# Kernel optimization log

Measured on AMD Instinct MI355X. Metric: run time of the kernel, lower is better.

The kernel has to match this reference:

```python
import math
import jax, jax.numpy as jnp
import numpy as np

S, H, D = 2048, 16, 128

def setup_inputs() -> dict:
    key = jax.random.key(0)
    kq, kk, kv = jax.random.split(key, 3)
    Q = jax.random.normal(kq, (S, H, D), dtype=jnp.float32)
    K = jax.random.normal(kk, (S, H, D), dtype=jnp.float32)
    V = jax.random.normal(kv, (S, H, D), dtype=jnp.float32)
    return {"Q": Q, "K": K, "V": V}

def reference(Q, K, V):
    s, h, d = Q.shape
    # scores[i,h,j] = sum_d Q[i,h,d] * K[j,h,d]  (torch einsum 'ijk,kjl->ijl' with K.T)
    scores = jnp.einsum('ihd,jhd->ihj', Q, K) / np.float32(math.sqrt(d))
    # causal mask: y -= triu(inf, 1) broadcast over heads -> -inf above diagonal
    causal = jnp.triu(jnp.ones((s, s), dtype=bool), k=1)  # [S, S]
    scores = jnp.where(causal[:, None, :], -jnp.inf, scores)
    attn = jax.nn.softmax(scores, axis=2)  # softmax over keys (dim 2)
    # out[i,h,d] = sum_j attn[i,h,j] * V[j,h,d]
    return jnp.einsum('ihj,jhd->ihd', attn, V)
```

## Files before the change

### kernel.cpp

```cpp
#include <hip/hip_runtime.h>
#include <hip/hip_bf16.h>

#define S_LEN 2048
#define NH 16
#define HD 128
#define KBLK 64
#define SM_BOUND 14.0f

typedef short short8 __attribute__((ext_vector_type(8)));
typedef float f32x4 __attribute__((ext_vector_type(4)));

__device__ __forceinline__ ushort f2bf(float f) {
  union { float f; unsigned u; } v; v.f = f;
  unsigned u = v.u;
  return (ushort)((u + 0x7fffu + ((u >> 16) & 1u)) >> 16);
}

#define GLDS(gp, lp)                                                      \
  __builtin_amdgcn_global_load_lds(                                       \
      (const __attribute__((address_space(1))) void*)(gp),                \
      (__attribute__((address_space(3))) void*)(lp), 16, 0, 0)

__global__ __launch_bounds__(256)
void prep(const float* __restrict__ Kg, const float* __restrict__ Vg,
          ushort* __restrict__ Kb, ushort* __restrict__ Vb) {
  __shared__ ushort lt[64 * HD];
  const int tid = threadIdx.x;
  const int h = blockIdx.x & 15;
  const int j0 = (blockIdx.x >> 4) * 64;

#pragma unroll
  for (int it = 0; it < 8; ++it) {
    int flat = it * 256 + tid;
    int r = flat >> 5, d4 = (flat & 31) * 4;
    float4 v = *(const float4*)(Kg + ((size_t)(j0 + r) * NH + h) * HD + d4);
    ushort4 b;
    b.x = f2bf(v.x); b.y = f2bf(v.y); b.z = f2bf(v.z); b.w = f2bf(v.w);
    *(ushort4*)(Kb + ((size_t)h * S_LEN + j0 + r) * HD + d4) = b;
  }
#pragma unroll
  for (int it = 0; it < 8; ++it) {
    int flat = it * 256 + tid;
    int r = flat >> 5, d4 = (flat & 31) * 4;
    float4 v = *(const float4*)(Vg + ((size_t)(j0 + r) * NH + h) * HD + d4);
    ushort4 b;
    b.x = f2bf(v.x); b.y = f2bf(v.y); b.z = f2bf(v.z); b.w = f2bf(v.w);
    *(ushort4*)(&lt[r * 128 + (d4 ^ ((r & 7) << 3))]) = b;
  }
  __syncthreads();
  const int d = tid >> 1, half = tid & 1;
  ushort vals[32];
#pragma unroll
  for (int j = 0; j < 32; ++j) {
    int jjj = half * 32 + j;
    vals[j] = lt[jjj * 128 + (d ^ ((jjj & 7) << 3))];
  }
  ushort* dst = Vb + ((size_t)h * HD + d) * S_LEN + j0 + half * 32;
#pragma unroll
  for (int q = 0; q < 4; ++q) {
    short8 w;
#pragma unroll
    for (int e = 0; e < 8; ++e) w[e] = (short)vals[q * 8 + e];
    *(short8*)(dst + q * 8) = w;
  }
}

__global__ __launch_bounds__(512, 2)
void attn_fwd6(const float* __restrict__ Qg, const ushort* __restrict__ Kb,
               const ushort* __restrict__ Vb, float* __restrict__ Og) {
  __shared__ ushort lds_k[3][KBLK * HD];
  __shared__ ushort lds_vt[3][HD * KBLK];
  __shared__ ushort lds_p[64 * 64];
  __shared__ float  lsc[2][4][2][16];

  const int tid = threadIdx.x;
  const int l   = tid & 63;
  const int wv  = tid >> 6;
  const int qf  = wv >> 2;
  const int kh  = wv & 3;
  const int dh  = wv & 3;
  const int lr  = l & 15;
  const int lg  = l >> 4;

  const int bid = blockIdx.x;
  const int h   = bid & 15;
  const int jj  = bid >> 4;
  const int qtA = 31 - jj;
  const int qbA = qtA * 64, qbB = jj * 64;

  const ushort* khp = Kb + (size_t)h * S_LEN * HD;
  const ushort* vhp = Vb + (size_t)h * HD * S_LEN;

  const int b0 = tid, b1 = 512 + tid;
  const int r0 = b0 >> 4, r1 = b1 >> 4;
  const int koff0 = r0 * 128 + (((b0 & 15) ^ (r0 & 7)) << 3);
  const int koff1 = r1 * 128 + (((b1 & 15) ^ (r1 & 7)) << 3);
  const int dd0 = b0 >> 3, dd1 = b1 >> 3;
  const int voff0 = dd0 * S_LEN + (((b0 & 7) ^ (dd0 & 7)) << 3);
  const int voff1 = dd1 * S_LEN + (((b1 & 7) ^ (dd1 & 7)) << 3);

  auto stage = [&](int buf, int kc) {
    const ushort* kbase = khp + (size_t)kc * (KBLK * HD);
    GLDS(kbase + koff0, &lds_k[buf][tid * 8]);
    GLDS(kbase + koff1, &lds_k[buf][4096 + tid * 8]);
    const ushort* vbase = vhp + (size_t)kc * KBLK;
    GLDS(vbase + voff0, &lds_vt[buf][tid * 8]);
    GLDS(vbase + voff1, &lds_vt[buf][4096 + tid * 8]);
  };

  const float scale = 0.08838834764831845f;
  short8 qfrA[2][4], qfrB[2][4];
  auto loadQ = [&](short8 (&dst)[2][4], int qb) {
#pragma unroll
    for (int qc = 0; qc < 2; ++qc) {
      const float* qsrc = Qg + ((size_t)(qb + qf * 32 + qc * 16 + lr) * NH + h) * HD;
#pragma unroll
      for (int dk = 0; dk < 4; ++dk) {
        float4 a = *(const float4*)(qsrc + dk * 32 + lg * 8);
        float4 b2 = *(const float4*)(qsrc + dk * 32 + lg * 8 + 4);
        short8 f;
        f[0] = (short)f2bf(a.x * scale);  f[1] = (short)f2bf(a.y * scale);
        f[2] = (short)f2bf(a.z * scale);  f[3] = (short)f2bf(a.w * scale);
        f[4] = (short)f2bf(b2.x * scale); f[5] = (short)f2bf(b2.y * scale);
        f[6] = (short)f2bf(b2.z * scale); f[7] = (short)f2bf(b2.w * scale);
        dst[qc][dk] = f;
      }
    }
  };
  loadQ(qfrA, qbA);
  loadQ(qfrB, qbB);

  f32x4 oacc[2][2];
#pragma unroll
  for (int qc = 0; qc < 2; ++qc)
#pragma unroll
    for (int dt = 0; dt < 2; ++dt) oacc[qc][dt] = (f32x4){0.f, 0.f, 0.f, 0.f};
  float l_run[2] = {0.f, 0.f};

  auto epilogue = [&](int qb) {
    float t0 = l_run[0], t1 = l_run[1];
    t0 += __shfl_xor(t0, 16, 64); t0 += __shfl_xor(t0, 32, 64);
    t1 += __shfl_xor(t1, 16, 64); t1 += __shfl_xor(t1, 32, 64);
    if (lg == 0) { lsc[qf][kh][0][lr] = t0; lsc[qf][kh][1][lr] = t1; }
    __syncthreads();
    float inv[2][4];
#pragma unroll
    for (int qc = 0; qc < 2; ++qc)
#pragma unroll
      for (int i = 0; i < 4; ++i) {
        int q15 = lg * 4 + i;
        float sl = (lsc[qf][0][qc][q15] + lsc[qf][1][qc][q15]) +
                   (lsc[qf][2][qc][q15] + lsc[qf][3][qc][q15]);
        inv[qc][i] = 1.0f / sl;
      }
#pragma unroll
    for (int qc = 0; qc < 2; ++qc)
#pragma unroll
      for (int dt = 0; dt < 2; ++dt)
#pragma unroll
        for (int i = 0; i < 4; ++i) {
          int qg = qb + qf * 32 + qc * 16 + lg * 4 + i;
          Og[((size_t)qg * NH + h) * HD + dh * 32 + dt * 16 + lr] =
              oacc[qc][dt][i] * inv[qc][i];
        }
  };

  stage(0, 0);
  stage(1, 1);

  for (int g = 0; g < 33; ++g) {
    if (g == 32) { asm volatile("s_waitcnt vmcnt(0)" ::: "memory"); }
    else         { asm volatile("s_waitcnt vmcnt(4)" ::: "memory"); }
    asm volatile("s_barrier" ::: "memory");
    if (g + 2 < 33) {
      int t = g + 2;
      stage(t % 3, (t <= qtA) ? t : (t - qtA - 1));
    }
    const int bI = g % 3;
    const ushort* lk = lds_k[bI];
    const ushort* lv = lds_vt[bI];
    const bool tB = (g > qtA);
    const int kc = tB ? (g - qtA - 1) : g;
    const int qb = tB ? qbB : qbA;

    f32x4 s0 = (f32x4){0.f, 0.f, 0.f, 0.f};
    f32x4 s1 = (f32x4){0.f, 0.f, 0.f, 0.f};
    const int krow = kh * 16 + lr;
    __builtin_amdgcn_s_setprio(1);
    if (!tB) {
#pragma unroll
      for (int dk = 0; dk < 4; ++dk) {
        short8 kf = *(const short8*)&lk[krow * 128 + ((dk * 32 + lg * 8) ^ ((lr & 7) << 3))];
        s0 = __builtin_amdgcn_mfma_f32_16x16x32_bf16(kf, qfrA[0][dk], s0, 0, 0, 0);
        s1 = __builtin_amdgcn_mfma_f32_16x16x32_bf16(kf, qfrA[1][dk], s1, 0, 0, 0);
      }
    } else {
#pragma unroll
      for (int dk = 0; dk < 4; ++dk) {
        short8 kf = *(const short8*)&lk[krow * 128 + ((dk * 32 + lg * 8) ^ ((lr & 7) << 3))];
        s0 = __builtin_amdgcn_mfma_f32_16x16x32_bf16(kf, qfrB[0][dk], s0, 0, 0, 0);
        s1 = __builtin_amdgcn_mfma_f32_16x16x32_bf16(kf, qfrB[1][dk], s1, 0, 0, 0);
      }
    }
    __builtin_amdgcn_s_setprio(0);

    float p0[4], p1[4];
    if (g == qtA || g == 32) {
      const int qg0 = qb + qf * 32 + lr;
#pragma unroll
      for (int i = 0; i < 4; ++i) {
        int kg = kc * 64 + kh * 16 + lg * 4 + i;
        float e0 = __expf(s0[i] - SM_BOUND);
        float e1 = __expf(s1[i] - SM_BOUND);
        p0[i] = (kg > qg0) ? 0.f : e0;
        p1[i] = (kg > qg0 + 16) ? 0.f : e1;
      }
    } else {
#pragma unroll
      for (int i = 0; i < 4; ++i) {
        p0[i] = __expf(s0[i] - SM_BOUND);
        p1[i] = __expf(s1[i] - SM_BOUND);
      }
    }
    l_run[0] += (p0[0] + p0[1]) + (p0[2] + p0[3]);
    l_run[1] += (p1[0] + p1[1]) + (p1[2] + p1[3]);

    {
      int q0 = qf * 32 + lr;
      int q1 = q0 + 16;
      unsigned w;
      asm("v_cvt_pk_bf16_f32 %0, %1, %2" : "=v"(w) : "v"(p0[0]), "v"(p0[1]));
      *(unsigned*)&lds_p[q0 * 64 + ((kh * 16 + lg * 4 + 0) ^ ((q0 & 7) << 3))] = w;
      asm("v_cvt_pk_bf16_f32 %0, %1, %2" : "=v"(w) : "v"(p0[2]), "v"(p0[3]));
      *(unsigned*)&lds_p[q0 * 64 + ((kh * 16 + lg * 4 + 2) ^ ((q0 & 7) << 3))] = w;
      asm("v_cvt_pk_bf16_f32 %0, %1, %2" : "=v"(w) : "v"(p1[0]), "v"(p1[1]));
      *(unsigned*)&lds_p[q1 * 64 + ((kh * 16 + lg * 4 + 0) ^ ((q1 & 7) << 3))] = w;
      asm("v_cvt_pk_bf16_f32 %0, %1, %2" : "=v"(w) : "v"(p1[2]), "v"(p1[3]));
      *(unsigned*)&lds_p[q1 * 64 + ((kh * 16 + lg * 4 + 2) ^ ((q1 & 7) << 3))] = w;
    }
    asm volatile("s_waitcnt lgkmcnt(0)" ::: "memory");
    asm volatile("s_barrier" ::: "memory");
    __builtin_amdgcn_sched_barrier(0);

    short8 pa0[2], pa1[2];
    {
      int q0 = qf * 32 + lr;
      int q1 = q0 + 16;
      pa0[0] = *(const short8*)&lds_p[q0 * 64 + ((lg * 8) ^ ((q0 & 7) << 3))];
      pa0[1] = *(const short8*)&lds_p[q0 * 64 + ((32 + lg * 8) ^ ((q0 & 7) << 3))];
      pa1[0] = *(const short8*)&lds_p[q1 * 64 + ((lg * 8) ^ ((q1 & 7) << 3))];
      pa1[1] = *(const short8*)&lds_p[q1 * 64 + ((32 + lg * 8) ^ ((q1 & 7) << 3))];
    }
    __builtin_amdgcn_s_setprio(1);
#pragma unroll
    for (int dt = 0; dt < 2; ++dt) {
      int d = dh * 32 + dt * 16 + lr;
#pragma unroll
      for (int ks = 0; ks < 2; ++ks) {
        short8 vf = *(const short8*)&lv[d * 64 + ((ks * 32 + lg * 8) ^ ((d & 7) << 3))];
        oacc[0][dt] = __builtin_amdgcn_mfma_f32_16x16x32_bf16(pa0[ks], vf, oacc[0][dt], 0, 0, 0);
        oacc[1][dt] = __builtin_amdgcn_mfma_f32_16x16x32_bf16(pa1[ks], vf, oacc[1][dt], 0, 0, 0);
      }
    }
    __builtin_amdgcn_s_setprio(0);

    if (g == qtA) {
      epilogue(qbA);
#pragma unroll
      for (int qc = 0; qc < 2; ++qc)
#pragma unroll
        for (int dt = 0; dt < 2; ++dt) oacc[qc][dt] = (f32x4){0.f, 0.f, 0.f, 0.f};
      l_run[0] = 0.f; l_run[1] = 0.f;
    }
  }
  epilogue(qbB);
}

__global__ __launch_bounds__(256, 2)
void attn_fwd_fb(const float* __restrict__ Qg, const float* __restrict__ Kg,
                 const float* __restrict__ Vg, float* __restrict__ Og) {
  __shared__ ushort lds_k[KBLK * HD];
  __shared__ ushort lds_vt[HD * KBLK];
  __shared__ ushort lds_p[4][16 * KBLK];

  const int tid = threadIdx.x;
  const int l  = tid & 63;
  const int wv = tid >> 6;
  const int lr = l & 15;
  const int lg = l >> 4;

  const int bid = blockIdx.x;
  const int h  = bid & 15;
  const int qi = bid >> 4;
  const int qt = (qi < 16) ? (31 - 2 * qi) : (2 * (qi - 16));
  const int qbase = qt * 64;

  short8 qf[4];
  {
    const float* qsrc = Qg + ((size_t)(qbase + wv * 16 + lr) * NH + h) * HD;
#pragma unroll
    for (int dk = 0; dk < 4; ++dk) {
      float4 a = *(const float4*)(qsrc + dk * 32 + lg * 8);
      float4 b = *(const float4*)(qsrc + dk * 32 + lg * 8 + 4);
      short8 f;
      f[0] = (short)f2bf(a.x); f[1] = (short)f2bf(a.y);
      f[2] = (short)f2bf(a.z); f[3] = (short)f2bf(a.w);
      f[4] = (short)f2bf(b.x); f[5] = (short)f2bf(b.y);
      f[6] = (short)f2bf(b.z); f[7] = (short)f2bf(b.w);
      qf[dk] = f;
    }
  }

  f32x4 oacc[8];
#pragma unroll
  for (int dt = 0; dt < 8; ++dt) oacc[dt] = (f32x4){0.f, 0.f, 0.f, 0.f};
  float l_run[4] = {0.f, 0.f, 0.f, 0.f};

  const float scale = 0.08838834764831845f;
  const int nch = qt + 1;

  for (int c = 0; c < nch; ++c) {
    const int k0 = c * KBLK;
    __syncthreads();
#pragma unroll
    for (int it = 0; it < 8; ++it) {
      int flat = (it * 256 + tid) * 4;
      int r = flat >> 7, d = flat & 127;
      float4 v = *(const float4*)(Kg + ((size_t)(k0 + r) * NH + h) * HD + d);
      int idx = (r * 128 + d) ^ ((r & 7) << 3);
      ushort4 b4;
      b4.x = f2bf(v.x); b4.y = f2bf(v.y); b4.z = f2bf(v.z); b4.w = f2bf(v.w);
      *(ushort4*)&lds_k[idx] = b4;
    }
#pragma unroll
    for (int it = 0; it < 8; ++it) {
      int d0 = wv * 32 + it * 4;
      float4 v = *(const float4*)(Vg + ((size_t)(k0 + l) * NH + h) * HD + d0);
      lds_vt[((d0 + 0) * 64 + l) ^ (((d0 + 0) & 7) << 3)] = f2bf(v.x);
      lds_vt[((d0 + 1) * 64 + l) ^ (((d0 + 1) & 7) << 3)] = f2bf(v.y);
      lds_vt[((d0 + 2) * 64 + l) ^ (((d0 + 2) & 7) << 3)] = f2bf(v.z);
      lds_vt[((d0 + 3) * 64 + l) ^ (((d0 + 3) & 7) << 3)] = f2bf(v.w);
    }
    __syncthreads();

    f32x4 sacc[4];
#pragma unroll
    for (int kc = 0; kc < 4; ++kc) {
      sacc[kc] = (f32x4){0.f, 0.f, 0.f, 0.f};
#pragma unroll
      for (int dk = 0; dk < 4; ++dk) {
        int row = kc * 16 + lr;
        int idx = (row * 128 + dk * 32 + lg * 8) ^ ((row & 7) << 3);
        short8 kf = *(const short8*)&lds_k[idx];
        sacc[kc] = __builtin_amdgcn_mfma_f32_16x16x32_bf16(qf[dk], kf, sacc[kc], 0, 0, 0);
      }
    }

    float p[4][4];
    if (c == qt) {
#pragma unroll
      for (int i = 0; i < 4; ++i) {
        int qg = qbase + wv * 16 + lg * 4 + i;
#pragma unroll
        for (int kc = 0; kc < 4; ++kc) {
          float e = __expf(sacc[kc][i] * scale - SM_BOUND);
          p[kc][i] = (k0 + kc * 16 + lr > qg) ? 0.f : e;
        }
      }
    } else {
#pragma unroll
      for (int i = 0; i < 4; ++i)
#pragma unroll
        for (int kc = 0; kc < 4; ++kc)
          p[kc][i] = __expf(sacc[kc][i] * scale - SM_BOUND);
    }
#pragma unroll
    for (int i = 0; i < 4; ++i)
      l_run[i] += (p[0][i] + p[1][i]) + (p[2][i] + p[3][i]);

#pragma unroll
    for (int kc = 0; kc < 4; ++kc)
#pragma unroll
      for (int i = 0; i < 4; ++i) {
        int row = lg * 4 + i, col = kc * 16 + lr;
        lds_p[wv][(row * 64 + col) ^ ((row & 7) << 3)] = f2bf(p[kc][i]);
      }
    asm volatile("s_waitcnt lgkmcnt(0)" ::: "memory");
    __builtin_amdgcn_sched_barrier(0);

    short8 pa[2];
#pragma unroll
    for (int ks = 0; ks < 2; ++ks) {
      int idx = (lr * 64 + ks * 32 + lg * 8) ^ ((lr & 7) << 3);
      pa[ks] = *(const short8*)&lds_p[wv][idx];
    }

#pragma unroll
    for (int dt = 0; dt < 8; ++dt) {
#pragma unroll
      for (int ks = 0; ks < 2; ++ks) {
        int d = dt * 16 + lr;
        int idx = (d * 64 + ks * 32 + lg * 8) ^ ((d & 7) << 3);
        short8 vf = *(const short8*)&lds_vt[idx];
        oacc[dt] = __builtin_amdgcn_mfma_f32_16x16x32_bf16(pa[ks], vf, oacc[dt], 0, 0, 0);
      }
    }
  }

#pragma unroll
  for (int mk = 1; mk <= 8; mk <<= 1)
#pragma unroll
    for (int i = 0; i < 4; ++i)
      l_run[i] += __shfl_xor(l_run[i], mk, 64);
  float inv[4];
#pragma unroll
  for (int i = 0; i < 4; ++i) inv[i] = 1.0f / l_run[i];
#pragma unroll
  for (int dt = 0; dt < 8; ++dt)
#pragma unroll
    for (int i = 0; i < 4; ++i) {
      int qg = qbase + wv * 16 + lg * 4 + i;
      Og[((size_t)qg * NH + h) * HD + dt * 16 + lr] = oacc[dt][i] * inv[i];
    }
}

extern "C" void kernel_launch(void* const* d_in, const int* in_sizes, int n_in,
                              void* d_out, int out_size, void* d_ws, size_t ws_size,
                              hipStream_t stream) {
  (void)in_sizes; (void)n_in; (void)out_size;
  const float* Q = (const float*)d_in[0];
  const float* K = (const float*)d_in[1];
  const float* V = (const float*)d_in[2];
  float* O = (float*)d_out;

  const size_t elems = (size_t)S_LEN * NH * HD;
  const size_t need = 2 * elems * sizeof(ushort);
  if (ws_size >= need) {
    ushort* Kb = (ushort*)d_ws;
    ushort* Vb = Kb + elems;
    prep<<<dim3(512), dim3(256), 0, stream>>>(K, V, Kb, Vb);
    attn_fwd6<<<dim3(256), dim3(512), 0, stream>>>(Q, Kb, Vb, O);
  } else {
    attn_fwd_fb<<<dim3(512), dim3(256), 0, stream>>>(Q, K, V, O);
  }
}
```

Baseline: 64.36 us.

## Double key block to 128 and restructure K/V staging pipeline

Raises the key block from 64 to 128 rows, so each wave computes a 32x32 score tile per step and the paired-tile loop drops from 33 to 17 iterations. K stays double-buffered in LDS while V becomes single-buffered; its next block is issued after the PV MFMAs finish, and the P scratch grows to 64x128. The aim is to cut per-iteration barrier, wait and softmax overhead and to get more MFMA work per sync. The cost is more masked work on diagonal chunks, V load latency that may no longer be hidden, and higher LDS use.

```diff
diff --git a/kernel.cpp b/kernel.cpp
--- a/kernel.cpp
+++ b/kernel.cpp
@@ -4,11 +4,13 @@
 #define S_LEN 2048
 #define NH 16
 #define HD 128
-#define KBLK 64
+#define KBLK 128
 #define SM_BOUND 14.0f
 
 typedef short short8 __attribute__((ext_vector_type(8)));
 typedef float f32x4 __attribute__((ext_vector_type(4)));
+
+#define MFMA32(a, b, c) __builtin_amdgcn_mfma_f32_16x16x32_bf16(a, b, c, 0, 0, 0)
 
 __device__ __forceinline__ ushort f2bf(float f) {
   union { float f; unsigned u; } v; v.f = f;
@@ -66,11 +68,11 @@
 }
 
 __global__ __launch_bounds__(512, 2)
-void attn_fwd6(const float* __restrict__ Qg, const ushort* __restrict__ Kb,
+void attn_fwd8(const float* __restrict__ Qg, const ushort* __restrict__ Kb,
                const ushort* __restrict__ Vb, float* __restrict__ Og) {
-  __shared__ ushort lds_k[3][KBLK * HD];
-  __shared__ ushort lds_vt[3][HD * KBLK];
-  __shared__ ushort lds_p[64 * 64];
+  __shared__ ushort lds_k[2][KBLK * HD];
+  __shared__ ushort lds_vt[HD * KBLK];
+  __shared__ ushort lds_p[64 * KBLK];
   __shared__ float  lsc[2][4][2][16];
 
   const int tid = threadIdx.x;
@@ -87,26 +89,33 @@
   const int jj  = bid >> 4;
   const int qtA = 31 - jj;
   const int qbA = qtA * 64, qbB = jj * 64;
+  const int nchA = (qtA >> 1) + 1;
+  const int nch  = 17;
 
   const ushort* khp = Kb + (size_t)h * S_LEN * HD;
   const ushort* vhp = Vb + (size_t)h * HD * S_LEN;
 
-  const int b0 = tid, b1 = 512 + tid;
-  const int r0 = b0 >> 4, r1 = b1 >> 4;
-  const int koff0 = r0 * 128 + (((b0 & 15) ^ (r0 & 7)) << 3);
-  const int koff1 = r1 * 128 + (((b1 & 15) ^ (r1 & 7)) << 3);
-  const int dd0 = b0 >> 3, dd1 = b1 >> 3;
-  const int voff0 = dd0 * S_LEN + (((b0 & 7) ^ (dd0 & 7)) << 3);
-  const int voff1 = dd1 * S_LEN + (((b1 & 7) ^ (dd1 & 7)) << 3);
-
-  auto stage = [&](int buf, int kc) {
+  int koff[4], voff[4];
+#pragma unroll
+  for (int i = 0; i < 4; ++i) {
+    int Dg = i * 512 + tid;
+    int r = Dg >> 4, gp = Dg & 15;
+    koff[i] = r * 128 + ((gp ^ (r & 7)) << 3);
+    voff[i] = r * S_LEN + ((gp ^ (r & 7)) << 3);
+  }
+  auto stageK = [&](int buf, int kc) {
     const ushort* kbase = khp + (size_t)kc * (KBLK * HD);
-    GLDS(kbase + koff0, &lds_k[buf][tid * 8]);
-    GLDS(kbase + koff1, &lds_k[buf][4096 + tid * 8]);
+#pragma unroll
+    for (int i = 0; i < 4; ++i)
+      GLDS(kbase + koff[i], &lds_k[buf][(i * 512 + tid) * 8]);
+  };
+  auto stageV = [&](int kc) {
     const ushort* vbase = vhp + (size_t)kc * KBLK;
-    GLDS(vbase + voff0, &lds_vt[buf][tid * 8]);
-    GLDS(vbase + voff1, &lds_vt[buf][4096 + tid * 8]);
+#pragma unroll
+    for (int i = 0; i < 4; ++i)
+      GLDS(vbase + voff[i], &lds_vt[(i * 512 + tid) * 8]);
   };
+  auto kc_of = [&](int g) { return (g < nchA) ? g : (g - nchA); };
 
   const float scale = 0.08838834764831845f;
   short8 qfrA[2][4], qfrB[2][4];
@@ -142,7 +151,8 @@
     t0 += __shfl_xor(t0, 16, 64); t0 += __shfl_xor(t0, 32, 64);
     t1 += __shfl_xor(t1, 16, 64); t1 += __shfl_xor(t1, 32, 64);
     if (lg == 0) { lsc[qf][kh][0][lr] = t0; lsc[qf][kh][1][lr] = t1; }
-    __syncthreads();
+    asm volatile("s_waitcnt lgkmcnt(0)" ::: "memory");
+    asm volatile("s_barrier" ::: "memory");
     float inv[2][4];
 #pragma unroll
     for (int qc = 0; qc < 2; ++qc)
@@ -163,108 +173,131 @@
           Og[((size_t)qg * NH + h) * HD + dh * 32 + dt * 16 + lr] =
               oacc[qc][dt][i] * inv[qc][i];
         }
+    asm volatile("s_barrier" ::: "memory");
   };
 
-  stage(0, 0);
-  stage(1, 1);
-
-  for (int g = 0; g < 33; ++g) {
-    if (g == 32) { asm volatile("s_waitcnt vmcnt(0)" ::: "memory"); }
-    else         { asm volatile("s_waitcnt vmcnt(4)" ::: "memory"); }
+  stageK(0, 0);
+  stageV(0);
+  stageK(1, (nchA > 1) ? 1 : 0);
+  asm volatile("s_waitcnt vmcnt(0)" ::: "memory");
+  __syncthreads();
+
+  for (int g = 0; g < nch; ++g) {
+    if (g + 1 < nch) { asm volatile("s_waitcnt vmcnt(4)" ::: "memory"); }
+    else             { asm volatile("s_waitcnt vmcnt(0)" ::: "memory"); }
     asm volatile("s_barrier" ::: "memory");
-    if (g + 2 < 33) {
-      int t = g + 2;
-      stage(t % 3, (t <= qtA) ? t : (t - qtA - 1));
-    }
-    const int bI = g % 3;
-    const ushort* lk = lds_k[bI];
-    const ushort* lv = lds_vt[bI];
-    const bool tB = (g > qtA);
-    const int kc = tB ? (g - qtA - 1) : g;
+
+    const int b = g & 1;
+    const ushort* lk = lds_k[b];
+    const bool tB = (g >= nchA);
+    const int kc = kc_of(g);
     const int qb = tB ? qbB : qbA;
-
-    f32x4 s0 = (f32x4){0.f, 0.f, 0.f, 0.f};
-    f32x4 s1 = (f32x4){0.f, 0.f, 0.f, 0.f};
-    const int krow = kh * 16 + lr;
+    const bool diag = (g == nchA - 1) || (g == nch - 1);
+
+    f32x4 s00 = (f32x4){0.f, 0.f, 0.f, 0.f};
+    f32x4 s01 = (f32x4){0.f, 0.f, 0.f, 0.f};
+    f32x4 s10 = (f32x4){0.f, 0.f, 0.f, 0.f};
+    f32x4 s11 = (f32x4){0.f, 0.f, 0.f, 0.f};
+    const int krow0 = kh * 32 + lr;
+    const int krow1 = krow0 + 16;
     __builtin_amdgcn_s_setprio(1);
     if (!tB) {
 #pragma unroll
       for (int dk = 0; dk < 4; ++dk) {
-        short8 kf = *(const short8*)&lk[krow * 128 + ((dk * 32 + lg * 8) ^ ((lr & 7) << 3))];
-        s0 = __builtin_amdgcn_mfma_f32_16x16x32_bf16(kf, qfrA[0][dk], s0, 0, 0, 0);
-        s1 = __builtin_amdgcn_mfma_f32_16x16x32_bf16(kf, qfrA[1][dk], s1, 0, 0, 0);
+        short8 kf0 = *(const short8*)&lk[krow0 * 128 + ((dk * 32 + lg * 8) ^ ((krow0 & 7) << 3))];
+        short8 kf1 = *(const short8*)&lk[krow1 * 128 + ((dk * 32 + lg * 8) ^ ((krow1 & 7) << 3))];
+        s00 = MFMA32(kf0, qfrA[0][dk], s00);
+        s01 = MFMA32(kf0, qfrA[1][dk], s01);
+        s10 = MFMA32(kf1, qfrA[0][dk], s10);
+        s11 = MFMA32(kf1, qfrA[1][dk], s11);
       }
     } else {
 #pragma unroll
       for (int dk = 0; dk < 4; ++dk) {
-        short8 kf = *(const short8*)&lk[krow * 128 + ((dk * 32 + lg * 8) ^ ((lr & 7) << 3))];
-        s0 = __builtin_amdgcn_mfma_f32_16x16x32_bf16(kf, qfrB[0][dk], s0, 0, 0, 0);
-        s1 = __builtin_amdgcn_mfma_f32_16x16x32_bf16(kf, qfrB[1][dk], s1, 0, 0, 0);
+        short8 kf0 = *(const short8*)&lk[krow0 * 128 + ((dk * 32 + lg * 8) ^ ((krow0 & 7) << 3))];
+        short8 kf1 = *(const short8*)&lk[krow1 * 128 + ((dk * 32 + lg * 8) ^ ((krow1 & 7) << 3))];
+        s00 = MFMA32(kf0, qfrB[0][dk], s00);
+        s01 = MFMA32(kf0, qfrB[1][dk], s01);
+        s10 = MFMA32(kf1, qfrB[0][dk], s10);
+        s11 = MFMA32(kf1, qfrB[1][dk], s11);
       }
     }
     __builtin_amdgcn_s_setprio(0);
 
-    float p0[4], p1[4];
-    if (g == qtA || g == 32) {
-      const int qg0 = qb + qf * 32 + lr;
+    float p[2][2][4];
+    if (diag) {
+#pragma unroll
+      for (int qc = 0; qc < 2; ++qc) {
+        int qg = qb + qf * 32 + qc * 16 + lr;
+#pragma unroll
+        for (int i = 0; i < 4; ++i) {
+          int kg0 = kc * 128 + kh * 32 + lg * 4 + i;
+          float e;
+          e = __expf((qc ? s01 : s00)[i] - SM_BOUND);
+          p[0][qc][i] = (kg0 > qg) ? 0.f : e;
+          e = __expf((qc ? s11 : s10)[i] - SM_BOUND);
+          p[1][qc][i] = (kg0 + 16 > qg) ? 0.f : e;
+        }
+      }
+    } else {
 #pragma unroll
       for (int i = 0; i < 4; ++i) {
-        int kg = kc * 64 + kh * 16 + lg * 4 + i;
-        float e0 = __expf(s0[i] - SM_BOUND);
-        float e1 = __expf(s1[i] - SM_BOUND);
-        p0[i] = (kg > qg0) ? 0.f : e0;
-        p1[i] = (kg > qg0 + 16) ? 0.f : e1;
-      }
-    } else {
-#pragma unroll
-      for (int i = 0; i < 4; ++i) {
-        p0[i] = __expf(s0[i] - SM_BOUND);
-        p1[i] = __expf(s1[i] - SM_BOUND);
-      }
-    }
-    l_run[0] += (p0[0] + p0[1]) + (p0[2] + p0[3]);
-    l_run[1] += (p1[0] + p1[1]) + (p1[2] + p1[3]);
-
-    {
-      int q0 = qf * 32 + lr;
-      int q1 = q0 + 16;
-      unsigned w;
-      asm("v_cvt_pk_bf16_f32 %0, %1, %2" : "=v"(w) : "v"(p0[0]), "v"(p0[1]));
-      *(unsigned*)&lds_p[q0 * 64 + ((kh * 16 + lg * 4 + 0) ^ ((q0 & 7) << 3))] = w;
-      asm("v_cvt_pk_bf16_f32 %0, %1, %2" : "=v"(w) : "v"(p0[2]), "v"(p0[3]));
-      *(unsigned*)&lds_p[q0 * 64 + ((kh * 16 + lg * 4 + 2) ^ ((q0 & 7) << 3))] = w;
-      asm("v_cvt_pk_bf16_f32 %0, %1, %2" : "=v"(w) : "v"(p1[0]), "v"(p1[1]));
-      *(unsigned*)&lds_p[q1 * 64 + ((kh * 16 + lg * 4 + 0) ^ ((q1 & 7) << 3))] = w;
-      asm("v_cvt_pk_bf16_f32 %0, %1, %2" : "=v"(w) : "v"(p1[2]), "v"(p1[3]));
-      *(unsigned*)&lds_p[q1 * 64 + ((kh * 16 + lg * 4 + 2) ^ ((q1 & 7) << 3))] = w;
+        p[0][0][i] = __expf(s00[i] - SM_BOUND);
+        p[0][1][i] = __expf(s01[i] - SM_BOUND);
+        p[1][0][i] = __expf(s10[i] - SM_BOUND);
+        p[1][1][i] = __expf(s11[i] - SM_BOUND);
+      }
+    }
+#pragma unroll
+    for (int qc = 0; qc < 2; ++qc)
+      l_run[qc] += ((p[0][qc][0] + p[0][qc][1]) + (p[0][qc][2] + p[0][qc][3])) +
+                   ((p[1][qc][0] + p[1][qc][1]) + (p[1][qc][2] + p[1][qc][3]));
+
+#pragma unroll
+    for (int qc = 0; qc < 2; ++qc) {
+      int q = qf * 32 + qc * 16 + lr;
+      int sw = (q & 7) << 3;
+#pragma unroll
+      for (int kcc = 0; kcc < 2; ++kcc) {
+        int kb = kh * 32 + kcc * 16 + lg * 4;
+        unsigned w;
+        asm("v_cvt_pk_bf16_f32 %0, %1, %2" : "=v"(w) : "v"(p[kcc][qc][0]), "v"(p[kcc][qc][1]));
+        *(unsigned*)&lds_p[q * 128 + ((((kb) >> 3 << 3) ^ sw) + (kb & 7))] = w;
+        asm("v_cvt_pk_bf16_f32 %0, %1, %2" : "=v"(w) : "v"(p[kcc][qc][2]), "v"(p[kcc][qc][3]));
+        *(unsigned*)&lds_p[q * 128 + ((((kb + 2) >> 3 << 3) ^ sw) + ((kb + 2) & 7))] = w;
+      }
     }
     asm volatile("s_waitcnt lgkmcnt(0)" ::: "memory");
     asm volatile("s_barrier" ::: "memory");
     __builtin_amdgcn_sched_barrier(0);
 
-    short8 pa0[2], pa1[2];
+    short8 pa0[4], pa1[4];
     {
-      int q0 = qf * 32 + lr;
-      int q1 = q0 + 16;
-      pa0[0] = *(const short8*)&lds_p[q0 * 64 + ((lg * 8) ^ ((q0 & 7) << 3))];
-      pa0[1] = *(const short8*)&lds_p[q0 * 64 + ((32 + lg * 8) ^ ((q0 & 7) << 3))];
-      pa1[0] = *(const short8*)&lds_p[q1 * 64 + ((lg * 8) ^ ((q1 & 7) << 3))];
-      pa1[1] = *(const short8*)&lds_p[q1 * 64 + ((32 + lg * 8) ^ ((q1 & 7) << 3))];
+      int q0 = qf * 32 + lr, q1 = q0 + 16;
+#pragma unroll
+      for (int ks = 0; ks < 4; ++ks) {
+        pa0[ks] = *(const short8*)&lds_p[q0 * 128 + (((ks * 4 + lg) ^ (q0 & 7)) << 3)];
+        pa1[ks] = *(const short8*)&lds_p[q1 * 128 + (((ks * 4 + lg) ^ (q1 & 7)) << 3)];
+      }
     }
     __builtin_amdgcn_s_setprio(1);
 #pragma unroll
     for (int dt = 0; dt < 2; ++dt) {
       int d = dh * 32 + dt * 16 + lr;
 #pragma unroll
-      for (int ks = 0; ks < 2; ++ks) {
-        short8 vf = *(const short8*)&lv[d * 64 + ((ks * 32 + lg * 8) ^ ((d & 7) << 3))];
-        oacc[0][dt] = __builtin_amdgcn_mfma_f32_16x16x32_bf16(pa0[ks], vf, oacc[0][dt], 0, 0, 0);
-        oacc[1][dt] = __builtin_amdgcn_mfma_f32_16x16x32_bf16(pa1[ks], vf, oacc[1][dt], 0, 0, 0);
+      for (int ks = 0; ks < 4; ++ks) {
+        short8 vf = *(const short8*)&lds_vt[d * 128 + (((ks * 4 + lg) ^ (d & 7)) << 3)];
+        oacc[0][dt] = MFMA32(pa0[ks], vf, oacc[0][dt]);
+        oacc[1][dt] = MFMA32(pa1[ks], vf, oacc[1][dt]);
       }
     }
     __builtin_amdgcn_s_setprio(0);
 
-    if (g == qtA) {
+    asm volatile("s_barrier" ::: "memory");
+    if (g + 1 < nch) stageV(kc_of(g + 1));
+    if (g + 2 < nch) stageK(b, kc_of(g + 2));
+
+    if (g == nchA - 1) {
       epilogue(qbA);
 #pragma unroll
       for (int qc = 0; qc < 2; ++qc)
@@ -279,9 +312,9 @@
 __global__ __launch_bounds__(256, 2)
 void attn_fwd_fb(const float* __restrict__ Qg, const float* __restrict__ Kg,
                  const float* __restrict__ Vg, float* __restrict__ Og) {
-  __shared__ ushort lds_k[KBLK * HD];
-  __shared__ ushort lds_vt[HD * KBLK];
-  __shared__ ushort lds_p[4][16 * KBLK];
+  __shared__ ushort lds_k[64 * HD];
+  __shared__ ushort lds_vt[HD * 64];
+  __shared__ ushort lds_p[4][16 * 64];
 
   const int tid = threadIdx.x;
   const int l  = tid & 63;
@@ -320,7 +353,7 @@
   const int nch = qt + 1;
 
   for (int c = 0; c < nch; ++c) {
-    const int k0 = c * KBLK;
+    const int k0 = c * 64;
     __syncthreads();
 #pragma unroll
     for (int it = 0; it < 8; ++it) {
@@ -352,7 +385,7 @@
         int row = kc * 16 + lr;
         int idx = (row * 128 + dk * 32 + lg * 8) ^ ((row & 7) << 3);
         short8 kf = *(const short8*)&lds_k[idx];
-        sacc[kc] = __builtin_amdgcn_mfma_f32_16x16x32_bf16(qf[dk], kf, sacc[kc], 0, 0, 0);
+        sacc[kc] = MFMA32(qf[dk], kf, sacc[kc]);
       }
     }
 
@@ -402,7 +435,7 @@
         int d = dt * 16 + lr;
         int idx = (d * 64 + ks * 32 + lg * 8) ^ ((d & 7) << 3);
         short8 vf = *(const short8*)&lds_vt[idx];
-        oacc[dt] = __builtin_amdgcn_mfma_f32_16x16x32_bf16(pa[ks], vf, oacc[dt], 0, 0, 0);
+        oacc[dt] = MFMA32(pa[ks], vf, oacc[dt]);
       }
     }
   }
@@ -439,7 +472,7 @@
     ushort* Kb = (ushort*)d_ws;
     ushort* Vb = Kb + elems;
     prep<<<dim3(512), dim3(256), 0, stream>>>(K, V, Kb, Vb);
-    attn_fwd6<<<dim3(256), dim3(512), 0, stream>>>(Q, Kb, Vb, O);
+    attn_fwd8<<<dim3(256), dim3(512), 0, stream>>>(Q, Kb, Vb, O);
   } else {
     attn_fwd_fb<<<dim3(512), dim3(256), 0, stream>>>(Q, K, V, O);
   }
```

After: 60.14 us. 6.6% less time.
